# Optimization experiments

Measured on AMD Instinct MI355X. Metric: run time of the kernel, lower is better.

The kernel has to match this reference:

```python
import jax, jax.numpy as jnp
import numpy as np

T, E, D = 16384, 16, 2048
CAPACITY = 2048  # per-expert capacity (supported_capacities=[2048])
TOP_K = 2


def setup_inputs() -> dict:
    key = jax.random.key(0)
    k1, k2, k3 = jax.random.split(key, 3)
    in_flow = jax.random.normal(k1, (T, D), dtype=jnp.float32)
    # router scores and a realistic top-k multi-hot mask
    logits = jax.random.normal(k2, (T, E), dtype=jnp.float32)
    score = jax.nn.softmax(logits, axis=-1)
    _, topk_idx = jax.lax.top_k(logits, TOP_K)  # [T, TOP_K]
    hot_mask = jnp.zeros((T, E), jnp.int32).at[jnp.arange(T)[:, None], topk_idx].set(1)
    return {"in_flow": in_flow, "hot_mask": hot_mask, "score": score}


def reference(in_flow, hot_mask, score):
    """Capacity-based fused MoE dispatch (HomoFusedDispatchSF):
    1) per-expert local indices via column-wise cumsum of the multi-hot mask,
    2) capacity-clipped loads,
    3) gather tokens scaled by gate score into expert-local buffers [E*C, D].
    """
    hm = (hot_mask > 0).astype(jnp.int32)               # [T, E]
    local = jnp.cumsum(hm, axis=0) * hm                 # 1-based local index per (token, expert)
    loads = jnp.minimum(hm.sum(axis=0), CAPACITY)       # [E]
    pos = local - 1                                     # 0-based slot within expert buffer
    valid = (hm > 0) & (pos < CAPACITY)                 # capacity overflow -> token dropped
    sentinel = E * CAPACITY
    dst = jnp.where(valid, jnp.arange(E)[None, :] * CAPACITY + pos, sentinel).reshape(-1)  # [T*E]
    tok = jnp.broadcast_to(jnp.arange(T, dtype=jnp.int32)[:, None], (T, E)).reshape(-1)
    # invert the scatter: which source token feeds each output slot (T = empty)
    src_tok = jnp.full((sentinel + 1,), T, jnp.int32).at[dst].set(tok)[:sentinel]          # [E*C]
    gate = jnp.zeros((sentinel + 1,), score.dtype).at[dst].set(score.reshape(-1))[:sentinel]
    slot_valid = src_tok < T
    gathered = jnp.take(in_flow, jnp.minimum(src_tok, T - 1), axis=0)                      # [E*C, D]
    out = jnp.where(slot_valid[:, None], gathered * gate[:, None], jnp.zeros((), in_flow.dtype))
    return out, loads
```

## Files before the change

kernel.cpp:

```cpp
#include <hip/hip_runtime.h>
#include <hip/hip_bf16.h>

#define T_TOK 16384
#define E_EXP 16
#define CAP   2048
#define D_DIM 2048
#define NCHUNK (T_TOK / 256)

typedef float vf4 __attribute__((ext_vector_type(4)));

__global__ __launch_bounds__(256) void count_kernel(
    const int* __restrict__ hot_mask,
    int*       __restrict__ counts)
{
    const int chunk = blockIdx.x;
    const int tid   = threadIdx.x;
    const int t     = chunk * 256 + tid;
    const int lane  = tid & 63;
    const int wv    = tid >> 6;

    const int4* row = (const int4*)(hot_mask + (size_t)t * E_EXP);
    int4 r0 = row[0], r1 = row[1], r2 = row[2], r3 = row[3];
    int hm[16] = { r0.x > 0, r0.y > 0, r0.z > 0, r0.w > 0,
                   r1.x > 0, r1.y > 0, r1.z > 0, r1.w > 0,
                   r2.x > 0, r2.y > 0, r2.z > 0, r2.w > 0,
                   r3.x > 0, r3.y > 0, r3.z > 0, r3.w > 0 };

    __shared__ int wcnt[4][16];
    #pragma unroll
    for (int e = 0; e < 16; ++e) {
        unsigned long long m = __ballot(hm[e]);
        if (lane == 0) wcnt[wv][e] = __popcll(m);
    }
    __syncthreads();
    if (tid < 16)
        counts[chunk * E_EXP + tid] =
            wcnt[0][tid] + wcnt[1][tid] + wcnt[2][tid] + wcnt[3][tid];
}

__global__ __launch_bounds__(64) void scan_kernel(
    const int* __restrict__ counts,
    int*       __restrict__ chunk_off,
    int*       __restrict__ loads_i,
    float*     __restrict__ loads_out)
{
    const int e    = blockIdx.x;
    const int lane = threadIdx.x;
    const int c    = counts[lane * E_EXP + e];
    int incl = c;
    #pragma unroll
    for (int off = 1; off < 64; off <<= 1) {
        int n = __shfl_up(incl, off, 64);
        if (lane >= off) incl += n;
    }
    chunk_off[lane * E_EXP + e] = incl - c;
    if (lane == 63) {
        int ld = incl < CAP ? incl : CAP;
        loads_i[e]   = ld;
        loads_out[e] = (float)ld;
    }
}

__global__ __launch_bounds__(256) void fill_kernel(
    const int*   __restrict__ hot_mask,
    const float* __restrict__ score,
    const int*   __restrict__ chunk_off,
    int*         __restrict__ src_tok,
    float*       __restrict__ gate)
{
    const int chunk = blockIdx.x;
    const int tid   = threadIdx.x;
    const int t     = chunk * 256 + tid;
    const int lane  = tid & 63;
    const int wv    = tid >> 6;

    const int4* mrow = (const int4*)(hot_mask + (size_t)t * E_EXP);
    int4 r0 = mrow[0], r1 = mrow[1], r2 = mrow[2], r3 = mrow[3];
    int hm[16] = { r0.x > 0, r0.y > 0, r0.z > 0, r0.w > 0,
                   r1.x > 0, r1.y > 0, r1.z > 0, r1.w > 0,
                   r2.x > 0, r2.y > 0, r2.z > 0, r2.w > 0,
                   r3.x > 0, r3.y > 0, r3.z > 0, r3.w > 0 };

    const float4* srow = (const float4*)(score + (size_t)t * E_EXP);
    float4 s0 = srow[0], s1 = srow[1], s2 = srow[2], s3 = srow[3];
    float sc[16] = { s0.x, s0.y, s0.z, s0.w, s1.x, s1.y, s1.z, s1.w,
                     s2.x, s2.y, s2.z, s2.w, s3.x, s3.y, s3.z, s3.w };

    __shared__ int wcnt[4][16];
    int before[16];
    const unsigned long long lmask = (1ULL << lane) - 1ULL;
    #pragma unroll
    for (int e = 0; e < 16; ++e) {
        unsigned long long m = __ballot(hm[e]);
        before[e] = __popcll(m & lmask);
        if (lane == 0) wcnt[wv][e] = __popcll(m);
    }
    __syncthreads();

    #pragma unroll
    for (int e = 0; e < 16; ++e) {
        if (hm[e]) {
            int woff = 0;
            for (int w = 0; w < 4; ++w) if (w < wv) woff += wcnt[w][e];
            const int pos = chunk_off[chunk * E_EXP + e] + woff + before[e];
            if (pos < CAP) {
                src_tok[e * CAP + pos] = t;
                gate[e * CAP + pos]    = sc[e];
            }
        }
    }
}

__global__ __launch_bounds__(256) void gather_scale_kernel(
    const float* __restrict__ in_flow,
    const int*   __restrict__ src_tok,
    const float* __restrict__ gate,
    const int*   __restrict__ loads_i,
    float*       __restrict__ out)
{
    const int slot = blockIdx.x;
    const int e    = slot >> 11;
    const int s    = slot & (CAP - 1);
    const int tid  = threadIdx.x;
    vf4* orow = (vf4*)(out + (size_t)slot * D_DIM);

    if (s < loads_i[e]) {
        const int   tok = src_tok[slot];
        const float g   = gate[slot];
        const vf4* irow = (const vf4*)(in_flow + (size_t)tok * D_DIM);
        vf4 v0 = irow[tid];
        vf4 v1 = irow[tid + 256];
        v0 *= g;
        v1 *= g;
        __builtin_nontemporal_store(v0, orow + tid);
        __builtin_nontemporal_store(v1, orow + tid + 256);
    } else {
        vf4 z = {0.f, 0.f, 0.f, 0.f};
        __builtin_nontemporal_store(z, orow + tid);
        __builtin_nontemporal_store(z, orow + tid + 256);
    }
}

extern "C" void kernel_launch(void* const* d_in, const int* in_sizes, int n_in,
                              void* d_out, int out_size, void* d_ws, size_t ws_size,
                              hipStream_t stream) {
    const float* in_flow  = (const float*)d_in[0];
    const int*   hot_mask = (const int*)d_in[1];
    const float* score    = (const float*)d_in[2];

    float* out       = (float*)d_out;
    float* loads_out = out + (size_t)E_EXP * CAP * D_DIM;

    char* ws = (char*)d_ws;
    int*   counts    = (int*)ws;                           ws += NCHUNK * E_EXP * sizeof(int);
    int*   chunk_off = (int*)ws;                           ws += NCHUNK * E_EXP * sizeof(int);
    int*   loads_i   = (int*)ws;                           ws += 64 * sizeof(int);
    int*   src_tok   = (int*)ws;                           ws += E_EXP * CAP * sizeof(int);
    float* gate      = (float*)ws;

    count_kernel<<<NCHUNK, 256, 0, stream>>>(hot_mask, counts);
    scan_kernel<<<E_EXP, 64, 0, stream>>>(counts, chunk_off, loads_i, loads_out);
    fill_kernel<<<NCHUNK, 256, 0, stream>>>(hot_mask, score, chunk_off, src_tok, gate);
    gather_scale_kernel<<<E_EXP * CAP, 256, 0, stream>>>(in_flow, src_tok, gate, loads_i, out);
}
```

Before: 380.3 us.

## Merge scan into fill and gather per source token, reading each row once

Folds the per-expert scan into the fill kernel: each block recomputes its own prefix from the chunk counts, which removes one launch. The fill now records each token's two destination slots and gates instead of an inverted slot map. The gather switches from one block per output slot to one block per source token, so each input row is read once and written to both of its destinations. A separate group of blocks zero-fills the unused slots after each expert's load. This cuts input reads roughly in half and removes a kernel, but it assumes at most two experts per token, which holds for top-2 masks only.

```diff
diff --git a/kernel.cpp b/kernel.cpp
--- a/kernel.cpp
+++ b/kernel.cpp
@@ -1,11 +1,11 @@
 #include <hip/hip_runtime.h>
-#include <hip/hip_bf16.h>
 
 #define T_TOK 16384
 #define E_EXP 16
 #define CAP   2048
 #define D_DIM 2048
 #define NCHUNK (T_TOK / 256)
+#define NZERO  128
 
 typedef float vf4 __attribute__((ext_vector_type(4)));
 
@@ -38,41 +38,40 @@
             wcnt[0][tid] + wcnt[1][tid] + wcnt[2][tid] + wcnt[3][tid];
 }
 
-__global__ __launch_bounds__(64) void scan_kernel(
-    const int* __restrict__ counts,
-    int*       __restrict__ chunk_off,
-    int*       __restrict__ loads_i,
-    float*     __restrict__ loads_out)
-{
-    const int e    = blockIdx.x;
-    const int lane = threadIdx.x;
-    const int c    = counts[lane * E_EXP + e];
-    int incl = c;
-    #pragma unroll
-    for (int off = 1; off < 64; off <<= 1) {
-        int n = __shfl_up(incl, off, 64);
-        if (lane >= off) incl += n;
-    }
-    chunk_off[lane * E_EXP + e] = incl - c;
-    if (lane == 63) {
-        int ld = incl < CAP ? incl : CAP;
-        loads_i[e]   = ld;
-        loads_out[e] = (float)ld;
-    }
-}
-
-__global__ __launch_bounds__(256) void fill_kernel(
+__global__ __launch_bounds__(256) void scanfill_kernel(
     const int*   __restrict__ hot_mask,
     const float* __restrict__ score,
-    const int*   __restrict__ chunk_off,
-    int*         __restrict__ src_tok,
-    float*       __restrict__ gate)
+    const int*   __restrict__ counts,
+    int*         __restrict__ dst2,
+    float*       __restrict__ g2,
+    int*         __restrict__ loads_i,
+    float*       __restrict__ loads_out)
 {
     const int chunk = blockIdx.x;
     const int tid   = threadIdx.x;
     const int t     = chunk * 256 + tid;
     const int lane  = tid & 63;
     const int wv    = tid >> 6;
+
+    __shared__ int s_off[16];
+    __shared__ int wcnt[4][16];
+
+    if (tid < 16) {
+        const int e = tid;
+        int off = 0, tot = 0;
+        #pragma unroll 8
+        for (int c = 0; c < NCHUNK; ++c) {
+            const int v = counts[c * E_EXP + e];
+            off += (c < chunk) ? v : 0;
+            tot += v;
+        }
+        s_off[e] = off;
+        if (chunk == 0) {
+            const int ld = tot < CAP ? tot : CAP;
+            loads_i[e]   = ld;
+            loads_out[e] = (float)ld;
+        }
+    }
 
     const int4* mrow = (const int4*)(hot_mask + (size_t)t * E_EXP);
     int4 r0 = mrow[0], r1 = mrow[1], r2 = mrow[2], r3 = mrow[3];
@@ -86,7 +85,6 @@
     float sc[16] = { s0.x, s0.y, s0.z, s0.w, s1.x, s1.y, s1.z, s1.w,
                      s2.x, s2.y, s2.z, s2.w, s3.x, s3.y, s3.z, s3.w };
 
-    __shared__ int wcnt[4][16];
     int before[16];
     const unsigned long long lmask = (1ULL << lane) - 1ULL;
     #pragma unroll
@@ -97,47 +95,67 @@
     }
     __syncthreads();
 
+    int   d0 = -1, d1 = -1;
+    float gg0 = 0.f, gg1 = 0.f;
+    int   k = 0;
     #pragma unroll
     for (int e = 0; e < 16; ++e) {
         if (hm[e]) {
             int woff = 0;
             for (int w = 0; w < 4; ++w) if (w < wv) woff += wcnt[w][e];
-            const int pos = chunk_off[chunk * E_EXP + e] + woff + before[e];
-            if (pos < CAP) {
-                src_tok[e * CAP + pos] = t;
-                gate[e * CAP + pos]    = sc[e];
-            }
+            const int pos  = s_off[e] + woff + before[e];
+            const int slot = (pos < CAP) ? e * CAP + pos : -1;
+            if (k == 0)      { d0 = slot; gg0 = sc[e]; }
+            else if (k == 1) { d1 = slot; gg1 = sc[e]; }
+            ++k;
         }
     }
+    ((int2*)dst2)[t]  = make_int2(d0, d1);
+    ((float2*)g2)[t]  = make_float2(gg0, gg1);
 }
 
-__global__ __launch_bounds__(256) void gather_scale_kernel(
+__global__ __launch_bounds__(256) void gather_kernel(
     const float* __restrict__ in_flow,
-    const int*   __restrict__ src_tok,
-    const float* __restrict__ gate,
+    const int*   __restrict__ dst2,
+    const float* __restrict__ g2,
     const int*   __restrict__ loads_i,
     float*       __restrict__ out)
 {
-    const int slot = blockIdx.x;
-    const int e    = slot >> 11;
-    const int s    = slot & (CAP - 1);
-    const int tid  = threadIdx.x;
-    vf4* orow = (vf4*)(out + (size_t)slot * D_DIM);
+    const int b   = blockIdx.x;
+    const int tid = threadIdx.x;
 
-    if (s < loads_i[e]) {
-        const int   tok = src_tok[slot];
-        const float g   = gate[slot];
-        const vf4* irow = (const vf4*)(in_flow + (size_t)tok * D_DIM);
-        vf4 v0 = irow[tid];
-        vf4 v1 = irow[tid + 256];
-        v0 *= g;
-        v1 *= g;
-        __builtin_nontemporal_store(v0, orow + tid);
-        __builtin_nontemporal_store(v1, orow + tid + 256);
-    } else {
-        vf4 z = {0.f, 0.f, 0.f, 0.f};
-        __builtin_nontemporal_store(z, orow + tid);
-        __builtin_nontemporal_store(z, orow + tid + 256);
+    if (b < NZERO) {
+        const int e = b >> 3, p = b & 7;
+        const int ld = loads_i[e];
+        const vf4 z = {0.f, 0.f, 0.f, 0.f};
+        for (int s = ld + p; s < CAP; s += 8) {
+            vf4* o = (vf4*)(out + ((size_t)e * CAP + s) * D_DIM);
+            __builtin_nontemporal_store(z, o + tid);
+            __builtin_nontemporal_store(z, o + tid + 256);
+        }
+        return;
+    }
+
+    const int t  = b - NZERO;
+    const int d0 = dst2[2 * t];
+    const int d1 = dst2[2 * t + 1];
+    if (d0 < 0 && d1 < 0) return;
+
+    const vf4* irow = (const vf4*)(in_flow + (size_t)t * D_DIM);
+    vf4 v0 = __builtin_nontemporal_load(irow + tid);
+    vf4 v1 = __builtin_nontemporal_load(irow + tid + 256);
+
+    if (d0 >= 0) {
+        const float g = g2[2 * t];
+        vf4* o = (vf4*)(out + (size_t)d0 * D_DIM);
+        __builtin_nontemporal_store(v0 * g, o + tid);
+        __builtin_nontemporal_store(v1 * g, o + tid + 256);
+    }
+    if (d1 >= 0) {
+        const float g = g2[2 * t + 1];
+        vf4* o = (vf4*)(out + (size_t)d1 * D_DIM);
+        __builtin_nontemporal_store(v0 * g, o + tid);
+        __builtin_nontemporal_store(v1 * g, o + tid + 256);
     }
 }
 
@@ -152,14 +170,14 @@
     float* loads_out = out + (size_t)E_EXP * CAP * D_DIM;
 
     char* ws = (char*)d_ws;
-    int*   counts    = (int*)ws;                           ws += NCHUNK * E_EXP * sizeof(int);
-    int*   chunk_off = (int*)ws;                           ws += NCHUNK * E_EXP * sizeof(int);
-    int*   loads_i   = (int*)ws;                           ws += 64 * sizeof(int);
-    int*   src_tok   = (int*)ws;                           ws += E_EXP * CAP * sizeof(int);
-    float* gate      = (float*)ws;
+    int*   counts  = (int*)ws;   ws += NCHUNK * E_EXP * sizeof(int);
+    int*   loads_i = (int*)ws;   ws += 64 * sizeof(int);
+    int*   dst2    = (int*)ws;   ws += (size_t)T_TOK * 2 * sizeof(int);
+    float* g2      = (float*)ws;
 
     count_kernel<<<NCHUNK, 256, 0, stream>>>(hot_mask, counts);
-    scan_kernel<<<E_EXP, 64, 0, stream>>>(counts, chunk_off, loads_i, loads_out);
-    fill_kernel<<<NCHUNK, 256, 0, stream>>>(hot_mask, score, chunk_off, src_tok, gate);
-    gather_scale_kernel<<<E_EXP * CAP, 256, 0, stream>>>(in_flow, src_tok, gate, loads_i, out);
+    scanfill_kernel<<<NCHUNK, 256, 0, stream>>>(hot_mask, score, counts,
+                                                dst2, g2, loads_i, loads_out);
+    gather_kernel<<<T_TOK + NZERO, 256, 0, stream>>>(in_flow, dst2, g2,
+                                                     loads_i, out);
 }
```

Measured after the change: 362.9 us. 4.6% less time.
